# Kernel tuning notes

Hardware: AMD Instinct MI355X
Metric: run time of the kernel (lower is better)

## Reference

```python
import jax, jax.numpy as jnp
import numpy as np

B, N, E, H = 4, 512, 512, 8
HD = E // H // 2            # 32; per-head value dim is 2*HD = 64
C_IN = 64                   # u_proj Conv2d in_channels
LAMBDA_INIT = 0.8 - 0.6 * float(np.exp(-0.3 * (28.0 / 28.0) * (1 - 1)))  # layer_idx=1, depth=28 -> 0.2
LN_EPS = 1e-5


def setup_inputs() -> dict:
    key = jax.random.key(0)
    ks = jax.random.split(key, 13)
    x = jax.random.normal(ks[0], (B, N, E), dtype=jnp.float32)
    u = jax.random.normal(ks[1], (B, N, N, C_IN), dtype=jnp.float32)
    umask = jax.random.randint(ks[2], (B, N, N, 2 * H), 0, 2).astype(bool)
    s = 0.02
    v_w = jax.random.normal(ks[3], (E, E), dtype=jnp.float32) * s        # nn.Linear weight [out,in]
    out_w = jax.random.normal(ks[4], (E, E), dtype=jnp.float32) * s
    uproj_w = jax.random.normal(ks[5], (2 * H, C_IN), dtype=jnp.float32) * s  # 1x1 conv kernel
    uproj_b = jax.random.normal(ks[6], (2 * H,), dtype=jnp.float32) * s
    lq1 = jax.random.normal(ks[7], (E,), dtype=jnp.float32) * 0.1
    lk1 = jax.random.normal(ks[8], (E,), dtype=jnp.float32) * 0.1
    lq2 = jax.random.normal(ks[9], (E,), dtype=jnp.float32) * 0.1
    lk2 = jax.random.normal(ks[10], (E,), dtype=jnp.float32) * 0.1
    ln_w = jnp.ones((2 * HD,), dtype=jnp.float32)
    ln_b = jnp.zeros((2 * HD,), dtype=jnp.float32)
    return {"x": x, "u": u, "umask": umask, "v_w": v_w, "out_w": out_w,
            "uproj_w": uproj_w, "uproj_b": uproj_b,
            "lq1": lq1, "lk1": lk1, "lq2": lq2, "lk2": lk2,
            "ln_w": ln_w, "ln_b": ln_b}


def reference(x, u, umask, v_w, out_w, uproj_w, uproj_b, lq1, lk1, lq2, lk2, ln_w, ln_b):
    b, n, e = x.shape
    # v projection -> [B, H, N, 2*HD]
    v = jnp.einsum('bne,fe->bnf', x, v_w).reshape(b, n, H, 2 * HD).transpose(0, 2, 1, 3)
    # 1x1 conv on u: [B,N,N,C_IN] -> [B,N,N,2H]
    ue = jnp.einsum('bnmc,hc->bnmh', u, uproj_w) + uproj_b
    ue = jnp.where(umask, -jnp.inf, ue)
    # transpose(3,1): [B,N,N,2H] -> [B,2H,N,N]; softmax over last (key) axis
    aw = jax.nn.softmax(jnp.transpose(ue, (0, 3, 2, 1)), axis=-1)
    lam1 = jnp.exp(jnp.sum(lq1 * lk1))
    lam2 = jnp.exp(jnp.sum(lq2 * lk2))
    lam = lam1 - lam2 + LAMBDA_INIT
    aw = aw.reshape(b, H, 2, n, n)
    diff = aw[:, :, 0] - lam * aw[:, :, 1]          # [B,H,N,N]
    attn = jnp.einsum('bhnm,bhmd->bhnd', diff, v)   # [B,H,N,2HD]
    # sub-LayerNorm over last dim
    mu = jnp.mean(attn, axis=-1, keepdims=True)
    var = jnp.mean(jnp.square(attn - mu), axis=-1, keepdims=True)
    attn = (attn - mu) * jax.lax.rsqrt(var + LN_EPS) * ln_w + ln_b
    attn = attn.transpose(0, 2, 1, 3).reshape(b, n, e)
    return jnp.einsum('bne,fe->bnf', attn, out_w)
```

## Files before the change

kernel.cpp:

```cpp
#include <hip/hip_runtime.h>
#include <math.h>

typedef _Float16 f16x8 __attribute__((ext_vector_type(8)));
typedef _Float16 f16x4 __attribute__((ext_vector_type(4)));
typedef float    f32x4 __attribute__((ext_vector_type(4)));

constexpr int kB  = 4;
constexpr int kN  = 512;
constexpr int kE  = 512;
constexpr int kH  = 8;
constexpr int kH2 = 16;
constexpr int kC  = 64;
constexpr int kDV = 64;
constexpr float kLamInit = 0.2f;

__global__ __launch_bounds__(256) void prep2_kernel(
    const float* __restrict__ x, const float* __restrict__ vw,
    const float* __restrict__ ow, const int* __restrict__ umask,
    const float* __restrict__ lq1, const float* __restrict__ lk1,
    const float* __restrict__ lq2, const float* __restrict__ lk2,
    _Float16* __restrict__ x16, _Float16* __restrict__ w16v,
    _Float16* __restrict__ w16o, unsigned short* __restrict__ mbits,
    float* __restrict__ lam_out) {
  const int bid = blockIdx.x;
  if (bid < 1536) {
    const float* src; _Float16* dst; int base;
    if (bid < 1024)      { src = x;  dst = x16;  base = bid; }
    else if (bid < 1280) { src = vw; dst = w16v; base = bid - 1024; }
    else                 { src = ow; dst = w16o; base = bid - 1280; }
    const int i = base * 256 + threadIdx.x;
    const float4 v = ((const float4*)src)[i];
    union { _Float16 h[4]; uint2 u2; } P;
    P.h[0]=(_Float16)v.x; P.h[1]=(_Float16)v.y;
    P.h[2]=(_Float16)v.z; P.h[3]=(_Float16)v.w;
    *(uint2*)(dst + i * 4) = P.u2;
  } else if (bid == 1536) {
    if (threadIdx.x < 64) {
      float s1 = 0.f, s2 = 0.f;
      for (int i = threadIdx.x; i < kE; i += 64) { s1 += lq1[i]*lk1[i]; s2 += lq2[i]*lk2[i]; }
      #pragma unroll
      for (int o = 32; o; o >>= 1) { s1 += __shfl_xor(s1, o); s2 += __shfl_xor(s2, o); }
      if (threadIdx.x == 0) lam_out[0] = expf(s1) - expf(s2) + kLamInit;
    }
  } else {
    const int i = (bid - 1537) * 256 + threadIdx.x;
    const int4* src = (const int4*)(umask + (size_t)i * kH2);
    unsigned int w = 0;
    #pragma unroll
    for (int c = 0; c < 4; ++c) {
      const int4 m = src[c];
      w |= (m.x & 1) << (c * 4 + 0);
      w |= (m.y & 1) << (c * 4 + 1);
      w |= (m.z & 1) << (c * 4 + 2);
      w |= (m.w & 1) << (c * 4 + 3);
    }
    mbits[i] = (unsigned short)w;
  }
}

__global__ __launch_bounds__(256) void hgemmT_v(const _Float16* __restrict__ W16,
                                                const _Float16* __restrict__ X16,
                                                _Float16* __restrict__ Vt) {
  const int tid = threadIdx.x, lane = tid & 63, wv = tid >> 6;
  const int l15 = lane & 15, l4 = lane >> 4;
  const int f0 = blockIdx.y * 64 + wv * 16;
  const int n0 = blockIdx.x * 64;
  f32x4 acc[4] = {{0,0,0,0},{0,0,0,0},{0,0,0,0},{0,0,0,0}};
  const _Float16* Ap = W16 + (size_t)(f0 + l15) * kE + l4 * 8;
  const _Float16* Bp = X16 + (size_t)(n0 + l15) * kE + l4 * 8;
  for (int k0 = 0; k0 < kE; k0 += 32) {
    const f16x8 af = *(const f16x8*)(Ap + k0);
    #pragma unroll
    for (int t = 0; t < 4; ++t) {
      const f16x8 bf = *(const f16x8*)(Bp + (size_t)t * 16 * kE + k0);
      acc[t] = __builtin_amdgcn_mfma_f32_16x16x32_f16(af, bf, acc[t], 0, 0, 0);
    }
  }
  #pragma unroll
  for (int t = 0; t < 4; ++t)
    #pragma unroll
    for (int r = 0; r < 4; ++r) {
      const int f  = f0 + l4 * 4 + r;
      const int ng = n0 + t * 16 + l15;
      const int bb = ng >> 9, n = ng & 511;
      Vt[(((size_t)((bb * kH + (f >> 6)) * kDV) + (f & 63)) * kN) + n] = (_Float16)acc[t][r];
    }
}

__global__ __launch_bounds__(512, 4) void fused_attn8(
    const float* __restrict__ u, const unsigned short* __restrict__ mbits,
    const float* __restrict__ uw, const float* __restrict__ ub,
    const _Float16* __restrict__ Vt,
    _Float16* __restrict__ Opart, float* __restrict__ Spart) {
  __shared__ _Float16 P[16 * 648];
  __shared__ float S_lds[8][16][17];
  const int tid = threadIdx.x, lane = tid & 63, wv = tid >> 6;
  const int l15 = lane & 15, l4 = lane >> 4;
  const int qt = blockIdx.x, kh = blockIdx.y, b = blockIdx.z;
  const int q0 = qt * 16;
  const int kstart = kh * 128;

  f16x8 bfrag[2];
  #pragma unroll
  for (int ch = 0; ch < 2; ++ch) {
    const float* wp = uw + l15 * 64 + ch * 32 + l4 * 8;
    const float4 wa = *(const float4*)wp;
    const float4 wb = *(const float4*)(wp + 4);
    f16x8 bf;
    bf[0]=(_Float16)wa.x; bf[1]=(_Float16)wa.y; bf[2]=(_Float16)wa.z; bf[3]=(_Float16)wa.w;
    bf[4]=(_Float16)wb.x; bf[5]=(_Float16)wb.y; bf[6]=(_Float16)wb.z; bf[7]=(_Float16)wb.w;
    bfrag[ch] = bf;
  }
  const float bias = ub[l15];

  const unsigned short* mb0 = mbits + (size_t)(b * kN) * kN + q0 + l4 * 4;

  float s_acc[4] = {};
  f32x4 oacc[2][4];
  #pragma unroll
  for (int s = 0; s < 2; ++s)
    #pragma unroll
    for (int d = 0; d < 4; ++d) oacc[s][d] = (f32x4){0,0,0,0};

  unsigned long long pm[4];
  #pragma unroll
  for (int kk = 0; kk < 4; ++kk)
    pm[kk] = *(const unsigned long long*)(mb0 + (size_t)(kstart + wv * 4 + kk) * kN);

  for (int t = 0; t < 4; ++t) {
    const int k0 = kstart + t * 32;
    _Float16 vals[4][4];
    #pragma unroll
    for (int kk = 0; kk < 4; ++kk) {
      const int k = k0 + wv * 4 + kk;
      const float* up = u + (((size_t)(b * kN + k)) * kN + q0 + l15) * kC + l4 * 8;
      f32x4 acc = {0.f, 0.f, 0.f, 0.f};
      #pragma unroll
      for (int ch = 0; ch < 2; ++ch) {
        const float4 a0 = *(const float4*)(up + ch * 32);
        const float4 a1 = *(const float4*)(up + ch * 32 + 4);
        f16x8 af;
        af[0]=(_Float16)a0.x; af[1]=(_Float16)a0.y; af[2]=(_Float16)a0.z; af[3]=(_Float16)a0.w;
        af[4]=(_Float16)a1.x; af[5]=(_Float16)a1.y; af[6]=(_Float16)a1.z; af[7]=(_Float16)a1.w;
        acc = __builtin_amdgcn_mfma_f32_16x16x32_f16(af, bfrag[ch], acc, 0, 0, 0);
      }
      #pragma unroll
      for (int r = 0; r < 4; ++r) {
        const float e = ((pm[kk] >> (r * 16 + l15)) & 1ULL) ? 0.f : __expf(acc[r] + bias);
        s_acc[r] += e;
        vals[r][kk] = (_Float16)e;
      }
    }
    #pragma unroll
    for (int r = 0; r < 4; ++r) {
      union { _Float16 h[4]; uint2 u2; } PK;
      #pragma unroll
      for (int kk = 0; kk < 4; ++kk) PK.h[kk] = vals[r][kk];
      *(uint2*)&P[l15 * 648 + (l4 * 4 + r) * 40 + wv * 4] = PK.u2;
    }
    __syncthreads();
    if (t < 3) {
      #pragma unroll
      for (int kk = 0; kk < 4; ++kk)
        pm[kk] = *(const unsigned long long*)(mb0 + (size_t)(k0 + 32 + wv * 4 + kk) * kN);
    }
    f16x8 va[4];
    #pragma unroll
    for (int dt = 0; dt < 4; ++dt)
      va[dt] = *(const f16x8*)(Vt + (((size_t)((b * kH + wv) * kDV + dt * 16 + l15)) * kN) + k0 + l4 * 8);
    #pragma unroll
    for (int s = 0; s < 2; ++s) {
      const f16x8 pb = *(const f16x8*)&P[(wv * 2 + s) * 648 + l15 * 40 + l4 * 8];
      #pragma unroll
      for (int dt = 0; dt < 4; ++dt)
        oacc[s][dt] = __builtin_amdgcn_mfma_f32_16x16x32_f16(va[dt], pb, oacc[s][dt], 0, 0, 0);
    }
    __syncthreads();
  }

  #pragma unroll
  for (int r = 0; r < 4; ++r) S_lds[wv][l15][l4 * 4 + r] = s_acc[r];
  __syncthreads();
  const int blk = (b * 4 + kh) * 32 + qt;
  if (tid < 256) {
    const int h2 = tid >> 4, q = tid & 15;
    float S = 0.f;
    #pragma unroll
    for (int j = 0; j < 8; ++j) S += S_lds[j][h2][q];
    Spart[(size_t)blk * 256 + h2 * 16 + q] = S;
  }
  _Float16* ob = Opart + (size_t)blk * 16384;
  #pragma unroll
  for (int s = 0; s < 2; ++s)
    #pragma unroll
    for (int dt = 0; dt < 4; ++dt)
      #pragma unroll
      for (int r = 0; r < 4; ++r)
        ob[((size_t)(s * 8 + wv) * 64 + dt * 16 + l4 * 4 + r) * 16 + l15] =
            (_Float16)oacc[s][dt][r];
}

__global__ __launch_bounds__(256) void combine_out(
    const _Float16* __restrict__ Opart, const float* __restrict__ Spart,
    const float* __restrict__ lam_p, const float* __restrict__ ln_w,
    const float* __restrict__ ln_b, const _Float16* __restrict__ w16o,
    float* __restrict__ out) {
  __shared__ _Float16 a_lds[16][520];
  __shared__ float vsh[64][17];
  __shared__ float inv_sh[2][16];
  const int tid = threadIdx.x;
  const int fh = blockIdx.x, qt = blockIdx.y, b = blockIdx.z;
  const float lam = lam_p[0];

  for (int h = 0; h < 8; ++h) {
    if (tid < 32) {
      const int s = tid >> 4, q = tid & 15;
      float S = 0.f;
      #pragma unroll
      for (int kh = 0; kh < 4; ++kh)
        S += Spart[(size_t)((b * 4 + kh) * 32 + qt) * 256 + (h * 2 + s) * 16 + q];
      inv_sh[s][q] = (s ? lam : 1.0f) / S;
    }
    float a0[4] = {}, a1[4] = {};
    #pragma unroll
    for (int kh = 0; kh < 4; ++kh) {
      const size_t base = (size_t)((b * 4 + kh) * 32 + qt) * 16384;
      const f16x4 p0 = *(const f16x4*)(Opart + base + (size_t)(0 * 8 + h) * 1024 + tid * 4);
      const f16x4 p1 = *(const f16x4*)(Opart + base + (size_t)(1 * 8 + h) * 1024 + tid * 4);
      #pragma unroll
      for (int j = 0; j < 4; ++j) { a0[j] += (float)p0[j]; a1[j] += (float)p1[j]; }
    }
    __syncthreads();
    {
      const int d = tid >> 2, q0i = (tid & 3) * 4;
      #pragma unroll
      for (int j = 0; j < 4; ++j)
        vsh[d][q0i + j] = a0[j] * inv_sh[0][q0i + j] - a1[j] * inv_sh[1][q0i + j];
    }
    __syncthreads();
    const int q = tid >> 4, i = tid & 15;
    float vv[4], s1 = 0.f, s2 = 0.f;
    #pragma unroll
    for (int jj = 0; jj < 4; ++jj) {
      vv[jj] = vsh[i * 4 + jj][q];
      s1 += vv[jj]; s2 += vv[jj] * vv[jj];
    }
    #pragma unroll
    for (int o = 1; o < 16; o <<= 1) { s1 += __shfl_xor(s1, o); s2 += __shfl_xor(s2, o); }
    const float mu = s1 * (1.0f / kDV);
    const float var = s2 * (1.0f / kDV) - mu * mu;
    const float rstd = rsqrtf(var + 1e-5f);
    #pragma unroll
    for (int jj = 0; jj < 4; ++jj)
      a_lds[q][h * kDV + i * 4 + jj] =
          (_Float16)((vv[jj] - mu) * rstd * ln_w[i * 4 + jj] + ln_b[i * 4 + jj]);
  }
  __syncthreads();

  const int lane = tid & 63, wv = tid >> 6;
  const int l15 = lane & 15, l4 = lane >> 4;
  const int f0 = fh * 256 + wv * 64;
  f32x4 acc[4] = {{0,0,0,0},{0,0,0,0},{0,0,0,0},{0,0,0,0}};
  const _Float16* Wp = w16o + (size_t)(f0 + l15) * kE + l4 * 8;
  for (int k0 = 0; k0 < kE; k0 += 32) {
    const f16x8 af = *(const f16x8*)&a_lds[l15][k0 + l4 * 8];
    #pragma unroll
    for (int ft = 0; ft < 4; ++ft) {
      const f16x8 bf = *(const f16x8*)(Wp + (size_t)ft * 16 * kE + k0);
      acc[ft] = __builtin_amdgcn_mfma_f32_16x16x32_f16(af, bf, acc[ft], 0, 0, 0);
    }
  }
  #pragma unroll
  for (int ft = 0; ft < 4; ++ft)
    #pragma unroll
    for (int r = 0; r < 4; ++r)
      out[(size_t)(b * kN + qt * 16 + l4 * 4 + r) * kE + f0 + ft * 16 + l15] = acc[ft][r];
}

extern "C" void kernel_launch(void* const* d_in, const int* in_sizes, int n_in,
                              void* d_out, int out_size, void* d_ws, size_t ws_size,
                              hipStream_t stream) {
  const float* x     = (const float*)d_in[0];
  const float* u     = (const float*)d_in[1];
  const int*   umask = (const int*)d_in[2];
  const float* v_w   = (const float*)d_in[3];
  const float* out_w = (const float*)d_in[4];
  const float* uw    = (const float*)d_in[5];
  const float* ubias = (const float*)d_in[6];
  const float* lq1   = (const float*)d_in[7];
  const float* lk1   = (const float*)d_in[8];
  const float* lq2   = (const float*)d_in[9];
  const float* lk2   = (const float*)d_in[10];
  const float* ln_w  = (const float*)d_in[11];
  const float* ln_b  = (const float*)d_in[12];
  float* out = (float*)d_out;

  char* ws = (char*)d_ws;
  const size_t sz_half = (size_t)kB * kN * kE * 2;
  const size_t sz_w16  = (size_t)kE * kE * 2;
  const size_t sz_op   = (size_t)512 * 16384 * 2;
  const size_t sz_sp   = (size_t)512 * 256 * 4;
  const size_t sz_mb   = (size_t)kB * kN * kN * 2;
  const size_t off_x16 = 256;
  const size_t off_wv  = off_x16 + sz_half;
  const size_t off_wo  = off_wv + sz_w16;
  const size_t off_vt  = off_wo + sz_w16;
  const size_t off_op  = off_vt + sz_half;
  const size_t off_sp  = off_op + sz_op;
  const size_t off_mb  = off_sp + sz_sp;
  if (ws_size < off_mb + sz_mb) return;
  float*    lam   = (float*)(ws);
  _Float16* x16   = (_Float16*)(ws + off_x16);
  _Float16* w16v  = (_Float16*)(ws + off_wv);
  _Float16* w16o  = (_Float16*)(ws + off_wo);
  _Float16* Vt    = (_Float16*)(ws + off_vt);
  _Float16* Opart = (_Float16*)(ws + off_op);
  float*    Spart = (float*)(ws + off_sp);
  unsigned short* mbits = (unsigned short*)(ws + off_mb);

  prep2_kernel<<<dim3(5633), dim3(256), 0, stream>>>(
      x, v_w, out_w, umask, lq1, lk1, lq2, lk2, x16, w16v, w16o, mbits, lam);
  hgemmT_v<<<dim3(32, 8), dim3(256), 0, stream>>>(w16v, x16, Vt);
  fused_attn8<<<dim3(kN / 16, 4, kB), dim3(512), 0, stream>>>(
      u, mbits, uw, ubias, Vt, Opart, Spart);
  combine_out<<<dim3(2, kN / 16, kB), dim3(256), 0, stream>>>(
      Opart, Spart, lam, ln_w, ln_b, w16o, out);
}
```

Before: 111.2 us.

## Split attention waves into producer and consumer roles with double-buffered P tiles

```diff
diff --git a/kernel.cpp b/kernel.cpp
--- a/kernel.cpp
+++ b/kernel.cpp
@@ -87,117 +87,138 @@
     }
 }
 
-__global__ __launch_bounds__(512, 4) void fused_attn8(
+__global__ __launch_bounds__(512, 4) void fused_attn10(
     const float* __restrict__ u, const unsigned short* __restrict__ mbits,
     const float* __restrict__ uw, const float* __restrict__ ub,
     const _Float16* __restrict__ Vt,
     _Float16* __restrict__ Opart, float* __restrict__ Spart) {
-  __shared__ _Float16 P[16 * 648];
-  __shared__ float S_lds[8][16][17];
+  __shared__ _Float16 P[2][16 * 648];
+  __shared__ float S_lds[4][16][17];
   const int tid = threadIdx.x, lane = tid & 63, wv = tid >> 6;
   const int l15 = lane & 15, l4 = lane >> 4;
   const int qt = blockIdx.x, kh = blockIdx.y, b = blockIdx.z;
   const int q0 = qt * 16;
   const int kstart = kh * 128;
+  const int blk = (b * 4 + kh) * 32 + qt;
+  const bool producer = (wv < 4);
 
   f16x8 bfrag[2];
+  float bias = 0.f;
+  float s_acc[4] = {0.f, 0.f, 0.f, 0.f};
+  const unsigned short* mb0 = mbits + (size_t)(b * kN) * kN + q0 + l4 * 4;
+  const int hc = (wv & 3) * 2;
+  f32x4 oacc[2][2][4];
   #pragma unroll
-  for (int ch = 0; ch < 2; ++ch) {
-    const float* wp = uw + l15 * 64 + ch * 32 + l4 * 8;
-    const float4 wa = *(const float4*)wp;
-    const float4 wb = *(const float4*)(wp + 4);
-    f16x8 bf;
-    bf[0]=(_Float16)wa.x; bf[1]=(_Float16)wa.y; bf[2]=(_Float16)wa.z; bf[3]=(_Float16)wa.w;
-    bf[4]=(_Float16)wb.x; bf[5]=(_Float16)wb.y; bf[6]=(_Float16)wb.z; bf[7]=(_Float16)wb.w;
-    bfrag[ch] = bf;
-  }
-  const float bias = ub[l15];
-
-  const unsigned short* mb0 = mbits + (size_t)(b * kN) * kN + q0 + l4 * 4;
-
-  float s_acc[4] = {};
-  f32x4 oacc[2][4];
-  #pragma unroll
-  for (int s = 0; s < 2; ++s)
-    #pragma unroll
-    for (int d = 0; d < 4; ++d) oacc[s][d] = (f32x4){0,0,0,0};
-
-  unsigned long long pm[4];
-  #pragma unroll
-  for (int kk = 0; kk < 4; ++kk)
-    pm[kk] = *(const unsigned long long*)(mb0 + (size_t)(kstart + wv * 4 + kk) * kN);
+  for (int a = 0; a < 2; ++a)
+    #pragma unroll
+    for (int s = 0; s < 2; ++s)
+      #pragma unroll
+      for (int d = 0; d < 4; ++d) oacc[a][s][d] = (f32x4){0.f, 0.f, 0.f, 0.f};
+
+  if (producer) {
+    #pragma unroll
+    for (int ch = 0; ch < 2; ++ch) {
+      const float* wp = uw + l15 * 64 + ch * 32 + l4 * 8;
+      const float4 wa = *(const float4*)wp;
+      const float4 wb = *(const float4*)(wp + 4);
+      f16x8 bf;
+      bf[0]=(_Float16)wa.x; bf[1]=(_Float16)wa.y; bf[2]=(_Float16)wa.z; bf[3]=(_Float16)wa.w;
+      bf[4]=(_Float16)wb.x; bf[5]=(_Float16)wb.y; bf[6]=(_Float16)wb.z; bf[7]=(_Float16)wb.w;
+      bfrag[ch] = bf;
+    }
+    bias = ub[l15];
+  }
+
+  auto produce = [&](int t) {
+    const int kbase = kstart + t * 32 + wv * 8;
+    #pragma unroll
+    for (int half = 0; half < 2; ++half) {
+      _Float16 vals[4][4];
+      #pragma unroll
+      for (int kk = 0; kk < 4; ++kk) {
+        const int k = kbase + half * 4 + kk;
+        const unsigned long long pm =
+            *(const unsigned long long*)(mb0 + (size_t)k * kN);
+        const float* up = u + (((size_t)(b * kN + k)) * kN + q0 + l15) * kC + l4 * 8;
+        f32x4 acc = {0.f, 0.f, 0.f, 0.f};
+        #pragma unroll
+        for (int ch = 0; ch < 2; ++ch) {
+          const float4 a0 = *(const float4*)(up + ch * 32);
+          const float4 a1 = *(const float4*)(up + ch * 32 + 4);
+          f16x8 af;
+          af[0]=(_Float16)a0.x; af[1]=(_Float16)a0.y; af[2]=(_Float16)a0.z; af[3]=(_Float16)a0.w;
+          af[4]=(_Float16)a1.x; af[5]=(_Float16)a1.y; af[6]=(_Float16)a1.z; af[7]=(_Float16)a1.w;
+          acc = __builtin_amdgcn_mfma_f32_16x16x32_f16(af, bfrag[ch], acc, 0, 0, 0);
+        }
+        #pragma unroll
+        for (int r = 0; r < 4; ++r) {
+          const float e = ((pm >> (r * 16 + l15)) & 1ULL) ? 0.f : __expf(acc[r] + bias);
+          s_acc[r] += e;
+          vals[r][kk] = (_Float16)e;
+        }
+      }
+      #pragma unroll
+      for (int r = 0; r < 4; ++r) {
+        union { _Float16 h[4]; uint2 u2; } PK;
+        #pragma unroll
+        for (int kk = 0; kk < 4; ++kk) PK.h[kk] = vals[r][kk];
+        *(uint2*)&P[t & 1][l15 * 648 + (l4 * 4 + r) * 40 + wv * 8 + half * 4] = PK.u2;
+      }
+    }
+  };
+
+  if (producer) produce(0);
+  __syncthreads();
 
   for (int t = 0; t < 4; ++t) {
-    const int k0 = kstart + t * 32;
-    _Float16 vals[4][4];
-    #pragma unroll
-    for (int kk = 0; kk < 4; ++kk) {
-      const int k = k0 + wv * 4 + kk;
-      const float* up = u + (((size_t)(b * kN + k)) * kN + q0 + l15) * kC + l4 * 8;
-      f32x4 acc = {0.f, 0.f, 0.f, 0.f};
-      #pragma unroll
-      for (int ch = 0; ch < 2; ++ch) {
-        const float4 a0 = *(const float4*)(up + ch * 32);
-        const float4 a1 = *(const float4*)(up + ch * 32 + 4);
-        f16x8 af;
-        af[0]=(_Float16)a0.x; af[1]=(_Float16)a0.y; af[2]=(_Float16)a0.z; af[3]=(_Float16)a0.w;
-        af[4]=(_Float16)a1.x; af[5]=(_Float16)a1.y; af[6]=(_Float16)a1.z; af[7]=(_Float16)a1.w;
-        acc = __builtin_amdgcn_mfma_f32_16x16x32_f16(af, bfrag[ch], acc, 0, 0, 0);
+    if (producer) {
+      if (t < 3) produce(t + 1);
+    } else {
+      const int k0 = kstart + t * 32;
+      #pragma unroll
+      for (int hp = 0; hp < 2; ++hp) {
+        const int h = hc + hp;
+        f16x8 va[4];
+        #pragma unroll
+        for (int dt = 0; dt < 4; ++dt)
+          va[dt] = *(const f16x8*)(Vt + (((size_t)((b * kH + h) * kDV + dt * 16 + l15)) * kN)
+                                   + k0 + l4 * 8);
+        #pragma unroll
+        for (int s = 0; s < 2; ++s) {
+          const f16x8 pb = *(const f16x8*)&P[t & 1][(h * 2 + s) * 648 + l15 * 40 + l4 * 8];
+          #pragma unroll
+          for (int dt = 0; dt < 4; ++dt)
+            oacc[hp][s][dt] = __builtin_amdgcn_mfma_f32_16x16x32_f16(va[dt], pb, oacc[hp][s][dt], 0, 0, 0);
+        }
       }
-      #pragma unroll
-      for (int r = 0; r < 4; ++r) {
-        const float e = ((pm[kk] >> (r * 16 + l15)) & 1ULL) ? 0.f : __expf(acc[r] + bias);
-        s_acc[r] += e;
-        vals[r][kk] = (_Float16)e;
-      }
-    }
-    #pragma unroll
-    for (int r = 0; r < 4; ++r) {
-      union { _Float16 h[4]; uint2 u2; } PK;
-      #pragma unroll
-      for (int kk = 0; kk < 4; ++kk) PK.h[kk] = vals[r][kk];
-      *(uint2*)&P[l15 * 648 + (l4 * 4 + r) * 40 + wv * 4] = PK.u2;
     }
     __syncthreads();
-    if (t < 3) {
-      #pragma unroll
-      for (int kk = 0; kk < 4; ++kk)
-        pm[kk] = *(const unsigned long long*)(mb0 + (size_t)(k0 + 32 + wv * 4 + kk) * kN);
-    }
-    f16x8 va[4];
-    #pragma unroll
-    for (int dt = 0; dt < 4; ++dt)
-      va[dt] = *(const f16x8*)(Vt + (((size_t)((b * kH + wv) * kDV + dt * 16 + l15)) * kN) + k0 + l4 * 8);
-    #pragma unroll
-    for (int s = 0; s < 2; ++s) {
-      const f16x8 pb = *(const f16x8*)&P[(wv * 2 + s) * 648 + l15 * 40 + l4 * 8];
-      #pragma unroll
-      for (int dt = 0; dt < 4; ++dt)
-        oacc[s][dt] = __builtin_amdgcn_mfma_f32_16x16x32_f16(va[dt], pb, oacc[s][dt], 0, 0, 0);
-    }
-    __syncthreads();
-  }
-
-  #pragma unroll
-  for (int r = 0; r < 4; ++r) S_lds[wv][l15][l4 * 4 + r] = s_acc[r];
+  }
+
+  if (producer) {
+    #pragma unroll
+    for (int r = 0; r < 4; ++r) S_lds[wv][l15][l4 * 4 + r] = s_acc[r];
+  } else {
+    _Float16* ob = Opart + (size_t)blk * 16384;
+    #pragma unroll
+    for (int hp = 0; hp < 2; ++hp) {
+      const int h = hc + hp;
+      #pragma unroll
+      for (int s = 0; s < 2; ++s)
+        #pragma unroll
+        for (int dt = 0; dt < 4; ++dt)
+          #pragma unroll
+          for (int r = 0; r < 4; ++r)
+            ob[((size_t)(s * 8 + h) * 64 + dt * 16 + l4 * 4 + r) * 16 + l15] =
+                (_Float16)oacc[hp][s][dt][r];
+    }
+  }
   __syncthreads();
-  const int blk = (b * 4 + kh) * 32 + qt;
   if (tid < 256) {
     const int h2 = tid >> 4, q = tid & 15;
-    float S = 0.f;
-    #pragma unroll
-    for (int j = 0; j < 8; ++j) S += S_lds[j][h2][q];
+    const float S = S_lds[0][h2][q] + S_lds[1][h2][q] + S_lds[2][h2][q] + S_lds[3][h2][q];
     Spart[(size_t)blk * 256 + h2 * 16 + q] = S;
   }
-  _Float16* ob = Opart + (size_t)blk * 16384;
-  #pragma unroll
-  for (int s = 0; s < 2; ++s)
-    #pragma unroll
-    for (int dt = 0; dt < 4; ++dt)
-      #pragma unroll
-      for (int r = 0; r < 4; ++r)
-        ob[((size_t)(s * 8 + wv) * 64 + dt * 16 + l4 * 4 + r) * 16 + l15] =
-            (_Float16)oacc[s][dt][r];
 }
 
 __global__ __launch_bounds__(256) void combine_out(
@@ -321,7 +342,7 @@
   prep2_kernel<<<dim3(5633), dim3(256), 0, stream>>>(
       x, v_w, out_w, umask, lq1, lk1, lq2, lk2, x16, w16v, w16o, mbits, lam);
   hgemmT_v<<<dim3(32, 8), dim3(256), 0, stream>>>(w16v, x16, Vt);
-  fused_attn8<<<dim3(kN / 16, 4, kB), dim3(512), 0, stream>>>(
+  fused_attn10<<<dim3(kN / 16, 4, kB), dim3(512), 0, stream>>>(
       u, mbits, uw, ubias, Vt, Opart, Spart);
   combine_out<<<dim3(2, kN / 16, kB), dim3(256), 0, stream>>>(
       Opart, Spart, lam, ln_w, ln_b, w16o, out);
```

Measured after the change: 154.9 us. 1.39x slower.
